# Kernel optimization log

Measured on AMD Instinct MI355X. Metric: run time of the kernel, lower is better.

Reference implementation:

```python
import jax, jax.numpy as jnp
import numpy as np

B, N_HIST, N_PRED = 32, 12, 12
N_NODE, INPUT_DIM, OUTPUT_DIM = 325, 2, 1
HIDDEN, N_RNN_LAYERS = 256, 2
EDGE_DIM, NODE_DIM, ORDER = 2, 64, 2
K = ORDER * EDGE_DIM + 1  # number of concat blocks per GraphConv


def setup_inputs() -> dict:
    key = jax.random.key(0)
    ks = iter(jax.random.split(key, 40))

    def rn(shape, s=0.05):
        return jax.random.normal(next(ks), shape, jnp.float32) * s

    L, H = N_RNN_LAYERS, HIDDEN
    d = {}
    d['inputs'] = jax.random.normal(next(ks), (B, N_HIST, N_NODE, INPUT_DIM), jnp.float32)
    d['vertexes'] = rn((N_NODE, NODE_DIM), 1.0)
    d['arcs_w0'] = rn((2 * NODE_DIM, 4 * NODE_DIM)); d['arcs_b0'] = jnp.zeros((4 * NODE_DIM,), jnp.float32)
    d['arcs_w1'] = rn((4 * NODE_DIM, 4 * NODE_DIM)); d['arcs_b1'] = jnp.zeros((4 * NODE_DIM,), jnp.float32)
    d['arcs_w2'] = rn((4 * NODE_DIM, EDGE_DIM)); d['arcs_b2'] = jnp.zeros((EDGE_DIM,), jnp.float32)
    d['enc_pre_w0'] = rn((K * INPUT_DIM, H)); d['enc_pre_b0'] = jnp.zeros((H,), jnp.float32)
    d['enc_pre_w1'] = rn((K * H, H)); d['enc_pre_b1'] = jnp.zeros((H,), jnp.float32)
    d['enc_wih'] = rn((L, 4 * H, H)); d['enc_whh'] = rn((L, 4 * H, H))
    d['enc_bih'] = jnp.zeros((L, 4 * H), jnp.float32); d['enc_bhh'] = jnp.zeros((L, 4 * H), jnp.float32)
    d['dec_pre_w0'] = rn((K * OUTPUT_DIM, H)); d['dec_pre_b0'] = jnp.zeros((H,), jnp.float32)
    d['dec_pre_w1'] = rn((K * H, H)); d['dec_pre_b1'] = jnp.zeros((H,), jnp.float32)
    d['dec_wih'] = rn((L, 4 * H, H)); d['dec_whh'] = rn((L, 4 * H, H))
    d['dec_bih'] = jnp.zeros((L, 4 * H), jnp.float32); d['dec_bhh'] = jnp.zeros((L, 4 * H), jnp.float32)
    d['dec_post_w0'] = rn((K * H, H)); d['dec_post_b0'] = jnp.zeros((H,), jnp.float32)
    d['dec_post_w1'] = rn((K * H, H)); d['dec_post_b1'] = jnp.zeros((H,), jnp.float32)
    d['proj_w'] = rn((H, OUTPUT_DIM)); d['proj_b'] = jnp.zeros((OUTPUT_DIM,), jnp.float32)
    return d


def _graph_conv(x, supports, w, b):
    out = [x]
    for e in range(supports.shape[0]):
        a = supports[e]
        x1 = x
        for _ in range(ORDER):
            x1 = jnp.einsum('...vc,vw->...wc', x1, a)
            out.append(x1)
    return jnp.concatenate(out, -1) @ w + b


def _stacked_gc(x, supports, layers):
    for w, b in layers:
        x = jax.nn.relu(_graph_conv(x, supports, w, b))
    return x


def _lstm_step(x, h, c, wih, whh, bih, bhh):
    # x: [BN, H]; h, c: [L, BN, H]; torch gate order i, f, g, o
    new_h, new_c = [], []
    for l in range(N_RNN_LAYERS):
        gates = x @ wih[l].T + bih[l] + h[l] @ whh[l].T + bhh[l]
        i, f, g, o = jnp.split(gates, 4, axis=-1)
        cn = jax.nn.sigmoid(f) * c[l] + jax.nn.sigmoid(i) * jnp.tanh(g)
        hn = jax.nn.sigmoid(o) * jnp.tanh(cn)
        new_h.append(hn); new_c.append(cn)
        x = hn
    return x, jnp.stack(new_h), jnp.stack(new_c)


def _adaptive_supports(vertexes, arcs_w0, arcs_b0, arcs_w1, arcs_b1, arcs_w2, arcs_b2):
    n = vertexes.shape[0]
    src = jnp.broadcast_to(vertexes[None, :, :], (n, n, NODE_DIM))
    dst = jnp.broadcast_to(vertexes[:, None, :], (n, n, NODE_DIM))
    h = jnp.concatenate([src, dst], -1)
    h = jax.nn.leaky_relu(h @ arcs_w0 + arcs_b0)
    h = jax.nn.leaky_relu(h @ arcs_w1 + arcs_b1)
    adj = jnp.transpose(h @ arcs_w2 + arcs_b2, (2, 0, 1))  # [E, N, N]
    adj = jax.nn.relu(adj)
    adj = adj / jnp.maximum(jnp.sum(jnp.abs(adj), axis=2, keepdims=True), 1e-12)
    # FAITHFUL to source: adj is computed but the function returns identity.expand(adj.shape)
    return jnp.broadcast_to(jnp.eye(n, dtype=jnp.float32)[None], adj.shape)


def _forward(inputs, vertexes, arcs_w0, arcs_b0, arcs_w1, arcs_b1, arcs_w2, arcs_b2,
             enc_pre_w0, enc_pre_b0, enc_pre_w1, enc_pre_b1,
             enc_wih, enc_whh, enc_bih, enc_bhh,
             dec_pre_w0, dec_pre_b0, dec_pre_w1, dec_pre_b1,
             dec_wih, dec_whh, dec_bih, dec_bhh,
             dec_post_w0, dec_post_b0, dec_post_w1, dec_post_b1,
             proj_w, proj_b):
    b, t, n, _ = inputs.shape
    H, L = HIDDEN, N_RNN_LAYERS
    supports = _adaptive_supports(vertexes, arcs_w0, arcs_b0, arcs_w1, arcs_b1, arcs_w2, arcs_b2)

    # ---- encoding ----
    x = _stacked_gc(inputs, supports, [(enc_pre_w0, enc_pre_b0), (enc_pre_w1, enc_pre_b1)])  # [B,T,N,H]
    seq = jnp.transpose(x, (1, 0, 2, 3)).reshape(t, b * n, H)
    h0 = jnp.zeros((L, b * n, H), inputs.dtype)
    c0 = jnp.zeros((L, b * n, H), inputs.dtype)

    def enc_step(carry, xt):
        hh, cc = carry
        _, hh, cc = _lstm_step(xt, hh, cc, enc_wih, enc_whh, enc_bih, enc_bhh)
        return (hh, cc), None

    (h, c), _ = jax.lax.scan(enc_step, (h0, c0), seq)
    # NOTE: source calls torch.dropout but discards the result -> no-op; reproduced by omission.

    dec_in0 = jnp.zeros((b, n, OUTPUT_DIM), inputs.dtype)
    dec_pre = [(dec_pre_w0, dec_pre_b0), (dec_pre_w1, dec_pre_b1)]
    dec_post = [(dec_post_w0, dec_post_b0), (dec_post_w1, dec_post_b1)]

    def dec_step(carry, _):
        x, hh, cc = carry
        x = _stacked_gc(x, supports, dec_pre)                      # [B,N,H]
        xf, hh, cc = _lstm_step(x.reshape(b * n, H), hh, cc, dec_wih, dec_whh, dec_bih, dec_bhh)
        x = _stacked_gc(xf.reshape(b, n, H), supports, dec_post)   # [B,N,H]
        out = x @ proj_w + proj_b                                  # [B,N,out_dim]
        return (out, hh, cc), out

    _, outs = jax.lax.scan(dec_step, (dec_in0, h, c), None, length=N_PRED)
    return jnp.transpose(outs, (1, 0, 2, 3))  # [B, n_pred, N, output_dim]


def reference(inputs, vertexes, arcs_w0, arcs_b0, arcs_w1, arcs_b1, arcs_w2, arcs_b2,
              enc_pre_w0, enc_pre_b0, enc_pre_w1, enc_pre_b1,
              enc_wih, enc_whh, enc_bih, enc_bhh,
              dec_pre_w0, dec_pre_b0, dec_pre_w1, dec_pre_b1,
              dec_wih, dec_whh, dec_bih, dec_bhh,
              dec_post_w0, dec_post_b0, dec_post_w1, dec_post_b1,
              proj_w, proj_b):
    return _forward(inputs, vertexes, arcs_w0, arcs_b0, arcs_w1, arcs_b1, arcs_w2, arcs_b2,
                    enc_pre_w0, enc_pre_b0, enc_pre_w1, enc_pre_b1,
                    enc_wih, enc_whh, enc_bih, enc_bhh,
                    dec_pre_w0, dec_pre_b0, dec_pre_w1, dec_pre_b1,
                    dec_wih, dec_whh, dec_bih, dec_bhh,
                    dec_post_w0, dec_post_b0, dec_post_w1, dec_post_b1,
                    proj_w, proj_b)
```

## Files before the change

kernel.cpp:

```cpp
#include <hip/hip_runtime.h>
#include <math.h>

#define BATCH 32
#define NNODE 325
#define T_HIST 12
#define T_PRED 12
#define H 256
#define G4 1024
#define ROWS (BATCH*NNODE)
#define MPAD 10496

typedef __attribute__((ext_vector_type(8))) short bf16x8;
typedef __attribute__((ext_vector_type(4))) float f32x4;
typedef unsigned short ushort_t;
typedef unsigned int uint_t;

#define GLL16(gp, sp) __builtin_amdgcn_global_load_lds( \
    (const __attribute__((address_space(1))) void*)(gp), \
    (__attribute__((address_space(3))) void*)(sp), 16, 0, 0)

__device__ inline float bf2f(ushort_t u) { return __uint_as_float(((uint_t)u) << 16); }

__device__ inline void split2(float v, ushort_t& h, ushort_t& l) {
    uint_t b = __float_as_uint(v);
    uint_t hb = (b + 0x7fffu + ((b >> 16) & 1u)) & 0xffff0000u;
    h = (ushort_t)(hb >> 16);
    float r = v - __uint_as_float(hb);
    uint_t rb = __float_as_uint(r);
    l = (ushort_t)((rb + 0x7fffu + ((rb >> 16) & 1u)) >> 16);
}

__device__ inline float sigm(float x) {
    x = fminf(fmaxf(x, -30.f), 30.f);
    return 1.f / (1.f + __expf(-x));
}
__device__ inline float tanh_f(float x) {
    x = fminf(fmaxf(x, -15.f), 15.f);
    float e = __expf(2.f * x);
    return (e - 1.f) / (e + 1.f);
}

__global__ void collapse_kernel(const float* __restrict__ w, float* __restrict__ out,
                                int cin, int nblk) {
    int idx = blockIdx.x * blockDim.x + threadIdx.x;
    if (idx >= cin * H) return;
    int c = idx / H, h = idx % H;
    float s = 0.f;
    for (int k = 0; k < nblk; ++k) s += w[(size_t)(k * cin + c) * H + h];
    out[idx] = s;
}

__global__ void pack_big_kernel(const float* __restrict__ wih, const float* __restrict__ whh,
                                const float* __restrict__ bih, const float* __restrict__ bhh,
                                ushort_t* __restrict__ Bxh, ushort_t* __restrict__ Bxl,
                                ushort_t* __restrict__ Bhh, ushort_t* __restrict__ Bhl,
                                float* __restrict__ biasI) {
    int idx = blockIdx.x * blockDim.x + threadIdx.x;
    if (idx >= 32 * G4) return;
    int kg = idx >> 10, col = idx & 1023;
    int j = col >> 2, g = col & 3;
    int gcol = g * 256 + j;
    if (kg == 0) biasI[col] = bih[gcol] + bhh[gcol];
#pragma unroll
    for (int jj = 0; jj < 8; ++jj) {
        int k = kg * 8 + jj;
        ushort_t hh, ll;
        split2(wih[(size_t)gcol * H + k], hh, ll);
        Bxh[(size_t)idx * 8 + jj] = hh; Bxl[(size_t)idx * 8 + jj] = ll;
        split2(whh[(size_t)gcol * H + k], hh, ll);
        Bhh[(size_t)idx * 8 + jj] = hh; Bhl[(size_t)idx * 8 + jj] = ll;
    }
}

__global__ void pack_small_kernel(const float* __restrict__ w,
                                  ushort_t* __restrict__ Bh, ushort_t* __restrict__ Bl) {
    int idx = blockIdx.x * blockDim.x + threadIdx.x;
    if (idx >= 32 * H) return;
    int kg = idx >> 8, n = idx & 255;
#pragma unroll
    for (int jj = 0; jj < 8; ++jj) {
        int k = kg * 8 + jj;
        float s = 0.f;
        for (int blk = 0; blk < 5; ++blk) s += w[(size_t)(blk * H + k) * H + n];
        ushort_t hh, ll; split2(s, hh, ll);
        Bh[(size_t)idx * 8 + jj] = hh; Bl[(size_t)idx * 8 + jj] = ll;
    }
}

__global__ void enc_pre0_pk(const float* __restrict__ inp, const float* __restrict__ w,
                            const float* __restrict__ b, ushort_t* __restrict__ oh,
                            ushort_t* __restrict__ ol, int t) {
    int m = blockIdx.x * 256 + threadIdx.x;
    int kg = blockIdx.y;
    float ip0 = 0.f, ip1 = 0.f;
    if (m < ROWS) {
        int bb = m / NNODE, nn = m % NNODE;
        const float* ip = inp + (((size_t)bb * T_HIST + t) * NNODE + nn) * 2;
        ip0 = ip[0]; ip1 = ip[1];
    }
    union { ushort_t u[8]; bf16x8 v; } hc, lc;
#pragma unroll
    for (int jj = 0; jj < 8; ++jj) {
        int j = kg * 8 + jj;
        float v = (m < ROWS) ? fmaxf(ip0 * w[j] + ip1 * w[H + j] + b[j], 0.f) : 0.f;
        split2(v, hc.u[jj], lc.u[jj]);
    }
    size_t base = ((size_t)kg * MPAD + m) * 8;
    *(bf16x8*)&oh[base] = hc.v;
    *(bf16x8*)&ol[base] = lc.v;
}

__global__ void dec_pre0_pk(const float* __restrict__ y, const float* __restrict__ w,
                            const float* __restrict__ b, ushort_t* __restrict__ oh,
                            ushort_t* __restrict__ ol) {
    int m = blockIdx.x * 256 + threadIdx.x;
    int kg = blockIdx.y;
    float yv = y[m];
    union { ushort_t u[8]; bf16x8 v; } hc, lc;
#pragma unroll
    for (int jj = 0; jj < 8; ++jj) {
        int j = kg * 8 + jj;
        float v = fmaxf(yv * w[j] + b[j], 0.f);
        split2(v, hc.u[jj], lc.u[jj]);
    }
    size_t base = ((size_t)kg * MPAD + m) * 8;
    *(bf16x8*)&oh[base] = hc.v;
    *(bf16x8*)&ol[base] = lc.v;
}

template<bool GATES, int NSC, int HSC, int NB>
__global__ __launch_bounds__(256, 2) void gemm_k(
    const ushort_t* __restrict__ AxH, const ushort_t* __restrict__ AxL,
    const ushort_t* __restrict__ AhH, const ushort_t* __restrict__ AhL,
    int astrideX, int arowX, int astrideH,
    const ushort_t* __restrict__ BxH, const ushort_t* __restrict__ BxL,
    const ushort_t* __restrict__ BhH, const ushort_t* __restrict__ BhL,
    const float* __restrict__ bias, float* __restrict__ cst,
    ushort_t* __restrict__ OH, ushort_t* __restrict__ OL,
    int ostride, int nbx, int doSwz)
{
    __shared__ __align__(16) ushort_t As[2][2][4096];
    __shared__ __align__(16) ushort_t Bs[2][2][4096];

    int bid = blockIdx.x;
    if (doSwz) { int cpx = gridDim.x >> 3; bid = (bid & 7) * cpx + (bid >> 3); }
    const int bm = (bid / nbx) * 128, bn = (bid % nbx) * 128;
    const int tid = threadIdx.x, lane = tid & 63, wid = tid >> 6;
    const int wm = wid >> 1, wn = wid & 1;
    const int l15 = lane & 15, lk = lane >> 4;

    auto stageSC = [&](int s, int slot) {
        const ushort_t *Ah, *Al, *Bh, *Bl; int ck, astr, abase;
        if (s < HSC) { Ah = AxH; Al = AxL; Bh = BxH; Bl = BxL; ck = s; astr = astrideX; abase = arowX; }
        else         { Ah = AhH; Al = AhL; Bh = BhH; Bl = BhL; ck = s - HSC; astr = astrideH; abase = 0; }
#pragma unroll
        for (int q = 0; q < 2; ++q) {
            int ubase = (tid & 192) + q * 256;
            int u = ubase + lane;
            int kgl = u >> 7, rc = u & 127;
            size_t ga = ((size_t)(ck * 4 + kgl) * astr + abase + bm + rc) * 8;
            size_t gb = ((size_t)(ck * 4 + kgl) * NB + bn + rc) * 8;
            GLL16(Ah + ga, &As[slot][0][ubase * 8]);
            GLL16(Al + ga, &As[slot][1][ubase * 8]);
            GLL16(Bh + gb, &Bs[slot][0][ubase * 8]);
            GLL16(Bl + gb, &Bs[slot][1][ubase * 8]);
        }
    };

    f32x4 acc[4][4] = {};

    stageSC(0, 0);

#pragma unroll
    for (int s = 0; s < NSC; ++s) {
        __builtin_amdgcn_s_barrier();
        if (s + 1 < NSC) {
            stageSC(s + 1, (s + 1) & 1);
            asm volatile("s_waitcnt vmcnt(8)" ::: "memory");
        } else {
            asm volatile("s_waitcnt vmcnt(0)" ::: "memory");
        }
        __builtin_amdgcn_s_barrier();
        __builtin_amdgcn_sched_barrier(0);

        const int slot = s & 1;
        bf16x8 ah[4], al[4], bh[4], bl[4];
#pragma unroll
        for (int i = 0; i < 4; ++i) {
            int ea = (lk * 128 + wm * 64 + i * 16 + l15) * 8;
            ah[i] = *(const bf16x8*)&As[slot][0][ea];
            al[i] = *(const bf16x8*)&As[slot][1][ea];
            int eb = (lk * 128 + wn * 64 + i * 16 + l15) * 8;
            bh[i] = *(const bf16x8*)&Bs[slot][0][eb];
            bl[i] = *(const bf16x8*)&Bs[slot][1][eb];
        }
#pragma unroll
        for (int i = 0; i < 4; ++i)
#pragma unroll
            for (int j = 0; j < 4; ++j)
                acc[i][j] = __builtin_amdgcn_mfma_f32_16x16x32_bf16(bh[j], ah[i], acc[i][j], 0, 0, 0);
#pragma unroll
        for (int i = 0; i < 4; ++i)
#pragma unroll
            for (int j = 0; j < 4; ++j)
                acc[i][j] = __builtin_amdgcn_mfma_f32_16x16x32_bf16(bl[j], ah[i], acc[i][j], 0, 0, 0);
#pragma unroll
        for (int i = 0; i < 4; ++i)
#pragma unroll
            for (int j = 0; j < 4; ++j)
                acc[i][j] = __builtin_amdgcn_mfma_f32_16x16x32_bf16(bh[j], al[i], acc[i][j], 0, 0, 0);
    }

    if constexpr (GATES) {
        uint_t* Hs = (uint_t*)(&As[0][0][0]);
        const int jbase = (bn >> 2) + wn * 16;
#pragma unroll
        for (int jj = 0; jj < 4; ++jj) {
            float4 b4 = *(const float4*)&bias[bn + wn * 64 + jj * 16 + lk * 4];
            int j = jbase + jj * 4 + lk;
#pragma unroll
            for (int i = 0; i < 4; ++i) {
                int m = bm + wm * 64 + i * 16 + l15;
                float vi = acc[i][jj][0] + b4.x;
                float vf = acc[i][jj][1] + b4.y;
                float vg = acc[i][jj][2] + b4.z;
                float vo = acc[i][jj][3] + b4.w;
                float cold = cst[(size_t)j * MPAD + m];
                float cn = sigm(vf) * cold + sigm(vi) * tanh_f(vg);
                float hn = sigm(vo) * tanh_f(cn);
                cst[(size_t)j * MPAD + m] = cn;
                ushort_t hh, hl; split2(hn, hh, hl);
                Hs[(wm * 64 + i * 16 + l15) * 36 + wn * 16 + jj * 4 + lk] = ((uint_t)hh << 16) | hl;
            }
        }
        __syncthreads();
#pragma unroll
        for (int it = 0; it < 2; ++it) {
            int u = tid + it * 256;
            int mloc = u & 127, kgl = u >> 7;
            uint4 w0 = *(const uint4*)&Hs[mloc * 36 + kgl * 8];
            uint4 w1 = *(const uint4*)&Hs[mloc * 36 + kgl * 8 + 4];
            union { uint_t u2[4]; bf16x8 v; } hi, lo;
            hi.u2[0] = (w0.x >> 16) | (w0.y & 0xffff0000u);
            hi.u2[1] = (w0.z >> 16) | (w0.w & 0xffff0000u);
            hi.u2[2] = (w1.x >> 16) | (w1.y & 0xffff0000u);
            hi.u2[3] = (w1.z >> 16) | (w1.w & 0xffff0000u);
            lo.u2[0] = (w0.x & 0xffffu) | (w0.y << 16);
            lo.u2[1] = (w0.z & 0xffffu) | (w0.w << 16);
            lo.u2[2] = (w1.x & 0xffffu) | (w1.y << 16);
            lo.u2[3] = (w1.z & 0xffffu) | (w1.w << 16);
            size_t base = ((size_t)((bn >> 5) + kgl) * ostride + bm + mloc) * 8;
            *(bf16x8*)&OH[base] = hi.v;
            *(bf16x8*)&OL[base] = lo.v;
        }
    } else {
#pragma unroll
        for (int jj = 0; jj < 4; ++jj) {
            float4 b4 = *(const float4*)&bias[bn + wn * 64 + jj * 16 + lk * 4];
#pragma unroll
            for (int i = 0; i < 4; ++i) {
                float v0 = fmaxf(acc[i][jj][0] + b4.x, 0.f);
                float v1 = fmaxf(acc[i][jj][1] + b4.y, 0.f);
                float v2 = fmaxf(acc[i][jj][2] + b4.z, 0.f);
                float v3 = fmaxf(acc[i][jj][3] + b4.w, 0.f);
                ushort_t h0, h1, h2, h3, l0, l1, l2, l3;
                split2(v0, h0, l0); split2(v1, h1, l1);
                split2(v2, h2, l2); split2(v3, h3, l3);
                uint_t hu0 = (uint_t)h0 | ((uint_t)h1 << 16), hu1 = (uint_t)h2 | ((uint_t)h3 << 16);
                uint_t lu0 = (uint_t)l0 | ((uint_t)l1 << 16), lu1 = (uint_t)l2 | ((uint_t)l3 << 16);
                uint_t ph0 = (uint_t)__shfl_xor((int)hu0, 16, 64);
                uint_t ph1 = (uint_t)__shfl_xor((int)hu1, 16, 64);
                uint_t pl0 = (uint_t)__shfl_xor((int)lu0, 16, 64);
                uint_t pl1 = (uint_t)__shfl_xor((int)lu1, 16, 64);
                int kgg = ((bn + wn * 64 + jj * 16) >> 3) + (lk >> 1);
                size_t base = ((size_t)kgg * ostride + bm + wm * 64 + i * 16 + l15) * 8;
                union { uint_t u2[4]; bf16x8 v; } ch;
                if ((lk & 1) == 0) {
                    ch.u2[0] = hu0; ch.u2[1] = hu1; ch.u2[2] = ph0; ch.u2[3] = ph1;
                    *(bf16x8*)&OH[base] = ch.v;
                } else {
                    ch.u2[0] = pl0; ch.u2[1] = pl1; ch.u2[2] = lu0; ch.u2[3] = lu1;
                    *(bf16x8*)&OL[base] = ch.v;
                }
            }
        }
    }
}

__global__ void proj_kernel(const ushort_t* __restrict__ xh, const ushort_t* __restrict__ xl,
                            const float* __restrict__ pw, const float* __restrict__ pb,
                            float* __restrict__ y, float* __restrict__ out, int t) {
    int wid = threadIdx.x >> 6, lane = threadIdx.x & 63;
    int r = blockIdx.x * 4 + wid;
    if (r >= ROWS) return;
    const int kg = lane >> 1, sub = (lane & 1) * 4;
    size_t base = ((size_t)kg * MPAD + r) * 8 + sub;
    float s = 0.f;
#pragma unroll
    for (int q = 0; q < 4; ++q) {
        int k = kg * 8 + sub + q;
        s += (bf2f(xh[base + q]) + bf2f(xl[base + q])) * pw[k];
    }
#pragma unroll
    for (int off = 32; off > 0; off >>= 1) s += __shfl_down(s, off, 64);
    if (lane == 0) {
        float v = s + pb[0];
        y[r] = v;
        int bb = r / NNODE, n = r % NNODE;
        out[((size_t)bb * T_PRED + t) * NNODE + n] = v;
    }
}

static inline void gemm_big(const ushort_t* xH, const ushort_t* xL,
                            const ushort_t* hH, const ushort_t* hL,
                            ushort_t* const* B, const float* bias, float* c,
                            ushort_t* oH, ushort_t* oL, hipStream_t s) {
    gemm_k<true, 16, 8, 1024><<<656, 256, 0, s>>>(
        xH, xL, hH, hL, MPAD, 0, MPAD,
        B[0], B[1], B[2], B[3], bias, c, oH, oL, MPAD, 8, 1);
}
static inline void gemm_small(const ushort_t* aH, const ushort_t* aL,
                              const ushort_t* bH, const ushort_t* bL, const float* bias,
                              ushort_t* oH, ushort_t* oL, hipStream_t s) {
    gemm_k<false, 8, 8, 256><<<164, 256, 0, s>>>(
        aH, aL, nullptr, nullptr, MPAD, 0, MPAD,
        bH, bL, nullptr, nullptr, bias, nullptr, oH, oL, MPAD, 2, 0);
}

extern "C" void kernel_launch(void* const* d_in, const int* in_sizes, int n_in,
                              void* d_out, int out_size, void* d_ws, size_t ws_size,
                              hipStream_t stream) {
    (void)in_sizes; (void)n_in; (void)out_size; (void)ws_size;

    const float* inputs      = (const float*)d_in[0];
    const float* enc_pre_w0  = (const float*)d_in[8];
    const float* enc_pre_b0  = (const float*)d_in[9];
    const float* enc_pre_w1  = (const float*)d_in[10];
    const float* enc_pre_b1  = (const float*)d_in[11];
    const float* enc_wih     = (const float*)d_in[12];
    const float* enc_whh     = (const float*)d_in[13];
    const float* enc_bih     = (const float*)d_in[14];
    const float* enc_bhh     = (const float*)d_in[15];
    const float* dec_pre_w0  = (const float*)d_in[16];
    const float* dec_pre_b0  = (const float*)d_in[17];
    const float* dec_pre_w1  = (const float*)d_in[18];
    const float* dec_pre_b1  = (const float*)d_in[19];
    const float* dec_wih     = (const float*)d_in[20];
    const float* dec_whh     = (const float*)d_in[21];
    const float* dec_bih     = (const float*)d_in[22];
    const float* dec_bhh     = (const float*)d_in[23];
    const float* dec_post_w0 = (const float*)d_in[24];
    const float* dec_post_b0 = (const float*)d_in[25];
    const float* dec_post_w1 = (const float*)d_in[26];
    const float* dec_post_b1 = (const float*)d_in[27];
    const float* proj_w      = (const float*)d_in[28];
    const float* proj_b      = (const float*)d_in[29];
    float* out = (float*)d_out;

    char* wsb = (char*)d_ws;
    size_t off = 0;
    auto allocF = [&](size_t n) { float* p = (float*)(wsb + off); off += ((n * 4 + 15) & ~(size_t)15); return p; };
    auto allocU = [&](size_t n) { ushort_t* p = (ushort_t*)(wsb + off); off += ((n * 2 + 15) & ~(size_t)15); return p; };

    const size_t BIGW = (size_t)32 * G4 * 8;
    const size_t SMLW = (size_t)32 * H * 8;
    const size_t ACT  = (size_t)32 * MPAD * 8;

    ushort_t* eB0[4]; ushort_t* eB1[4]; ushort_t* dB0[4]; ushort_t* dB1[4];
    for (int q = 0; q < 4; ++q) eB0[q] = allocU(BIGW);
    for (int q = 0; q < 4; ++q) eB1[q] = allocU(BIGW);
    for (int q = 0; q < 4; ++q) dB0[q] = allocU(BIGW);
    for (int q = 0; q < 4; ++q) dB1[q] = allocU(BIGW);
    float* eBI0 = allocF(G4); float* eBI1 = allocF(G4);
    float* dBI0 = allocF(G4); float* dBI1 = allocF(G4);
    ushort_t* eP1h = allocU(SMLW); ushort_t* eP1l = allocU(SMLW);
    ushort_t* dP1h = allocU(SMLW); ushort_t* dP1l = allocU(SMLW);
    ushort_t* po0h = allocU(SMLW); ushort_t* po0l = allocU(SMLW);
    ushort_t* po1h = allocU(SMLW); ushort_t* po1l = allocU(SMLW);
    float* encW0eff = allocF(2 * H);
    float* decPre0eff = allocF(H);
    ushort_t* h0H[2]; ushort_t* h0L[2]; ushort_t* h1H[2]; ushort_t* h1L[2];
    for (int q = 0; q < 2; ++q) { h0H[q] = allocU(ACT); h0L[q] = allocU(ACT); }
    for (int q = 0; q < 2; ++q) { h1H[q] = allocU(ACT); h1L[q] = allocU(ACT); }
    float* c0 = allocF((size_t)H * MPAD);
    float* c1 = allocF((size_t)H * MPAD);
    ushort_t* xaH = allocU(ACT); ushort_t* xaL = allocU(ACT);
    ushort_t* xbH = allocU(ACT); ushort_t* xbL = allocU(ACT);
    float* y = allocF(MPAD);

    const size_t LOFF = (size_t)G4 * H;
    const int EW = 256;

    pack_big_kernel<<<128, EW, 0, stream>>>(enc_wih, enc_whh, enc_bih, enc_bhh,
                                            eB0[0], eB0[1], eB0[2], eB0[3], eBI0);
    pack_big_kernel<<<128, EW, 0, stream>>>(enc_wih + LOFF, enc_whh + LOFF, enc_bih + G4, enc_bhh + G4,
                                            eB1[0], eB1[1], eB1[2], eB1[3], eBI1);
    pack_big_kernel<<<128, EW, 0, stream>>>(dec_wih, dec_whh, dec_bih, dec_bhh,
                                            dB0[0], dB0[1], dB0[2], dB0[3], dBI0);
    pack_big_kernel<<<128, EW, 0, stream>>>(dec_wih + LOFF, dec_whh + LOFF, dec_bih + G4, dec_bhh + G4,
                                            dB1[0], dB1[1], dB1[2], dB1[3], dBI1);
    pack_small_kernel<<<32, EW, 0, stream>>>(enc_pre_w1, eP1h, eP1l);
    pack_small_kernel<<<32, EW, 0, stream>>>(dec_pre_w1, dP1h, dP1l);
    pack_small_kernel<<<32, EW, 0, stream>>>(dec_post_w0, po0h, po0l);
    pack_small_kernel<<<32, EW, 0, stream>>>(dec_post_w1, po1h, po1l);
    collapse_kernel<<<2, EW, 0, stream>>>(enc_pre_w0, encW0eff, 2, 5);
    collapse_kernel<<<1, EW, 0, stream>>>(dec_pre_w0, decPre0eff, 1, 5);

    for (int q = 0; q < 2; ++q) {
        hipMemsetAsync(h0H[q], 0, ACT * 2, stream); hipMemsetAsync(h0L[q], 0, ACT * 2, stream);
        hipMemsetAsync(h1H[q], 0, ACT * 2, stream); hipMemsetAsync(h1L[q], 0, ACT * 2, stream);
    }
    hipMemsetAsync(c0, 0, (size_t)H * MPAD * 4, stream);
    hipMemsetAsync(c1, 0, (size_t)H * MPAD * 4, stream);
    hipMemsetAsync(y, 0, (size_t)MPAD * 4, stream);

    const dim3 PG(MPAD / 256, 32);

    for (int t = 0; t < T_HIST; ++t) {
        int pr = t & 1;
        enc_pre0_pk<<<PG, EW, 0, stream>>>(inputs, encW0eff, enc_pre_b0, xaH, xaL, t);
        gemm_small(xaH, xaL, eP1h, eP1l, enc_pre_b1, xbH, xbL, stream);
        gemm_big(xbH, xbL, h0H[pr], h0L[pr], eB0, eBI0, c0, h0H[pr ^ 1], h0L[pr ^ 1], stream);
        gemm_big(h0H[pr ^ 1], h0L[pr ^ 1], h1H[pr], h1L[pr], eB1, eBI1, c1, h1H[pr ^ 1], h1L[pr ^ 1], stream);
    }

    for (int d = 0; d < T_PRED; ++d) {
        int pr = d & 1;
        dec_pre0_pk<<<PG, EW, 0, stream>>>(y, decPre0eff, dec_pre_b0, xaH, xaL);
        gemm_small(xaH, xaL, dP1h, dP1l, dec_pre_b1, xbH, xbL, stream);
        gemm_big(xbH, xbL, h0H[pr], h0L[pr], dB0, dBI0, c0, h0H[pr ^ 1], h0L[pr ^ 1], stream);
        gemm_big(h0H[pr ^ 1], h0L[pr ^ 1], h1H[pr], h1L[pr], dB1, dBI1, c1, h1H[pr ^ 1], h1L[pr ^ 1], stream);
        gemm_small(h1H[pr ^ 1], h1L[pr ^ 1], po0h, po0l, dec_post_b0, xaH, xaL, stream);
        gemm_small(xaH, xaL, po1h, po1l, dec_post_b1, xbH, xbL, stream);
        proj_kernel<<<(ROWS + 3) / 4, EW, 0, stream>>>(xbH, xbL, proj_w, proj_b, y, out, d);
    }
}
```

Baseline: 2.601 ms.

## Switch GEMM to 32x32x16 MFMA, narrow small-GEMM N tile, direct gate epilogue

The split-bf16 GEMM now uses 32x32x16 MFMA tiles in place of 16x16x32, which changes fragment loads and accumulator layout. The LSTM gate epilogue now writes h directly through lane shuffles and no longer goes through an LDS transpose with __syncthreads. The small GEMM uses a 64-wide N tile with double the blocks, swizzle enabled and min 3 waves per EU, to raise occupancy. The main cost targeted is MFMA issue overhead and the epilogue sync; s_setprio is added around the MFMA blocks. The risks are higher register pressure from 16-wide accumulators and partial (8-byte) stores in the non-gate epilogue.

New measurement: 2.777 ms. +6.8%, slower.

```diff
diff --git a/kernel.cpp b/kernel.cpp
--- a/kernel.cpp
+++ b/kernel.cpp
@@ -11,7 +11,7 @@
 #define MPAD 10496
 
 typedef __attribute__((ext_vector_type(8))) short bf16x8;
-typedef __attribute__((ext_vector_type(4))) float f32x4;
+typedef __attribute__((ext_vector_type(16))) float f32x16;
 typedef unsigned short ushort_t;
 typedef unsigned int uint_t;
 
@@ -128,46 +128,55 @@
     *(bf16x8*)&ol[base] = lc.v;
 }
 
-template<bool GATES, int NSC, int HSC, int NB>
-__global__ __launch_bounds__(256, 2) void gemm_k(
+template<bool GATES, int NSC, int HSC, int BNT, int NBG, int MINW>
+__global__ __launch_bounds__(256, MINW) void gemm_k(
     const ushort_t* __restrict__ AxH, const ushort_t* __restrict__ AxL,
     const ushort_t* __restrict__ AhH, const ushort_t* __restrict__ AhL,
-    int astrideX, int arowX, int astrideH,
     const ushort_t* __restrict__ BxH, const ushort_t* __restrict__ BxL,
     const ushort_t* __restrict__ BhH, const ushort_t* __restrict__ BhL,
     const float* __restrict__ bias, float* __restrict__ cst,
     ushort_t* __restrict__ OH, ushort_t* __restrict__ OL,
-    int ostride, int nbx, int doSwz)
+    int nbx, int doSwz)
 {
-    __shared__ __align__(16) ushort_t As[2][2][4096];
-    __shared__ __align__(16) ushort_t Bs[2][2][4096];
+    constexpr int ACH = 512;
+    constexpr int BCH = BNT * 4;
+    constexpr int BU = BCH / 256;
+    constexpr int JB = BNT / 64;
+    __shared__ __align__(16) ushort_t As[2][2][ACH * 8];
+    __shared__ __align__(16) ushort_t Bs[2][2][BCH * 8];
 
     int bid = blockIdx.x;
     if (doSwz) { int cpx = gridDim.x >> 3; bid = (bid & 7) * cpx + (bid >> 3); }
-    const int bm = (bid / nbx) * 128, bn = (bid % nbx) * 128;
+    const int bm = (bid / nbx) * 128, bn = (bid % nbx) * BNT;
     const int tid = threadIdx.x, lane = tid & 63, wid = tid >> 6;
     const int wm = wid >> 1, wn = wid & 1;
-    const int l15 = lane & 15, lk = lane >> 4;
+    const int l31 = lane & 31, hi = lane >> 5;
 
     auto stageSC = [&](int s, int slot) {
-        const ushort_t *Ah, *Al, *Bh, *Bl; int ck, astr, abase;
-        if (s < HSC) { Ah = AxH; Al = AxL; Bh = BxH; Bl = BxL; ck = s; astr = astrideX; abase = arowX; }
-        else         { Ah = AhH; Al = AhL; Bh = BhH; Bl = BhL; ck = s - HSC; astr = astrideH; abase = 0; }
+        const ushort_t *Ah, *Al, *Bh, *Bl; int ck;
+        if (s < HSC) { Ah = AxH; Al = AxL; Bh = BxH; Bl = BxL; ck = s; }
+        else         { Ah = AhH; Al = AhL; Bh = BhH; Bl = BhL; ck = s - HSC; }
 #pragma unroll
         for (int q = 0; q < 2; ++q) {
             int ubase = (tid & 192) + q * 256;
             int u = ubase + lane;
             int kgl = u >> 7, rc = u & 127;
-            size_t ga = ((size_t)(ck * 4 + kgl) * astr + abase + bm + rc) * 8;
-            size_t gb = ((size_t)(ck * 4 + kgl) * NB + bn + rc) * 8;
+            size_t ga = ((size_t)(ck * 4 + kgl) * MPAD + bm + rc) * 8;
             GLL16(Ah + ga, &As[slot][0][ubase * 8]);
             GLL16(Al + ga, &As[slot][1][ubase * 8]);
+        }
+#pragma unroll
+        for (int q = 0; q < BU; ++q) {
+            int ubase = (tid & 192) + q * 256;
+            int u = ubase + lane;
+            int kgl = u / BNT, nc = u % BNT;
+            size_t gb = ((size_t)(ck * 4 + kgl) * NBG + bn + nc) * 8;
             GLL16(Bh + gb, &Bs[slot][0][ubase * 8]);
             GLL16(Bl + gb, &Bs[slot][1][ubase * 8]);
         }
     };
 
-    f32x4 acc[4][4] = {};
+    f32x16 acc[2][JB] = {};
 
     stageSC(0, 0);
 
@@ -176,7 +185,8 @@
         __builtin_amdgcn_s_barrier();
         if (s + 1 < NSC) {
             stageSC(s + 1, (s + 1) & 1);
-            asm volatile("s_waitcnt vmcnt(8)" ::: "memory");
+            if constexpr (BU == 2) asm volatile("s_waitcnt vmcnt(8)" ::: "memory");
+            else                   asm volatile("s_waitcnt vmcnt(6)" ::: "memory");
         } else {
             asm volatile("s_waitcnt vmcnt(0)" ::: "memory");
         }
@@ -184,104 +194,120 @@
         __builtin_amdgcn_sched_barrier(0);
 
         const int slot = s & 1;
-        bf16x8 ah[4], al[4], bh[4], bl[4];
-#pragma unroll
-        for (int i = 0; i < 4; ++i) {
-            int ea = (lk * 128 + wm * 64 + i * 16 + l15) * 8;
-            ah[i] = *(const bf16x8*)&As[slot][0][ea];
-            al[i] = *(const bf16x8*)&As[slot][1][ea];
-            int eb = (lk * 128 + wn * 64 + i * 16 + l15) * 8;
-            bh[i] = *(const bf16x8*)&Bs[slot][0][eb];
-            bl[i] = *(const bf16x8*)&Bs[slot][1][eb];
-        }
-#pragma unroll
-        for (int i = 0; i < 4; ++i)
-#pragma unroll
-            for (int j = 0; j < 4; ++j)
-                acc[i][j] = __builtin_amdgcn_mfma_f32_16x16x32_bf16(bh[j], ah[i], acc[i][j], 0, 0, 0);
-#pragma unroll
-        for (int i = 0; i < 4; ++i)
-#pragma unroll
-            for (int j = 0; j < 4; ++j)
-                acc[i][j] = __builtin_amdgcn_mfma_f32_16x16x32_bf16(bl[j], ah[i], acc[i][j], 0, 0, 0);
-#pragma unroll
-        for (int i = 0; i < 4; ++i)
-#pragma unroll
-            for (int j = 0; j < 4; ++j)
-                acc[i][j] = __builtin_amdgcn_mfma_f32_16x16x32_bf16(bh[j], al[i], acc[i][j], 0, 0, 0);
+        bf16x8 afh[2][2], afl[2][2], bfh[2][JB], bfl[2][JB];
+#pragma unroll
+        for (int kh = 0; kh < 2; ++kh) {
+#pragma unroll
+            for (int i = 0; i < 2; ++i) {
+                int ca = ((2 * kh + hi) * 128 + wm * 64 + i * 32 + l31) * 8;
+                afh[kh][i] = *(const bf16x8*)&As[slot][0][ca];
+                afl[kh][i] = *(const bf16x8*)&As[slot][1][ca];
+            }
+#pragma unroll
+            for (int j = 0; j < JB; ++j) {
+                int cb = ((2 * kh + hi) * BNT + wn * (BNT / 2) + j * 32 + l31) * 8;
+                bfh[kh][j] = *(const bf16x8*)&Bs[slot][0][cb];
+                bfl[kh][j] = *(const bf16x8*)&Bs[slot][1][cb];
+            }
+        }
+        __builtin_amdgcn_s_setprio(1);
+#pragma unroll
+        for (int kh = 0; kh < 2; ++kh) {
+#pragma unroll
+            for (int i = 0; i < 2; ++i)
+#pragma unroll
+                for (int j = 0; j < JB; ++j)
+                    acc[i][j] = __builtin_amdgcn_mfma_f32_32x32x16_bf16(bfh[kh][j], afh[kh][i], acc[i][j], 0, 0, 0);
+#pragma unroll
+            for (int i = 0; i < 2; ++i)
+#pragma unroll
+                for (int j = 0; j < JB; ++j)
+                    acc[i][j] = __builtin_amdgcn_mfma_f32_32x32x16_bf16(bfl[kh][j], afh[kh][i], acc[i][j], 0, 0, 0);
+#pragma unroll
+            for (int i = 0; i < 2; ++i)
+#pragma unroll
+                for (int j = 0; j < JB; ++j)
+                    acc[i][j] = __builtin_amdgcn_mfma_f32_32x32x16_bf16(bfh[kh][j], afl[kh][i], acc[i][j], 0, 0, 0);
+        }
+        __builtin_amdgcn_s_setprio(0);
     }
 
     if constexpr (GATES) {
-        uint_t* Hs = (uint_t*)(&As[0][0][0]);
+        float4 b4[2][4];
+#pragma unroll
+        for (int jj = 0; jj < 2; ++jj)
+#pragma unroll
+            for (int q = 0; q < 4; ++q)
+                b4[jj][q] = *(const float4*)&bias[bn + wn * 64 + jj * 32 + 8 * q + 4 * hi];
         const int jbase = (bn >> 2) + wn * 16;
 #pragma unroll
-        for (int jj = 0; jj < 4; ++jj) {
-            float4 b4 = *(const float4*)&bias[bn + wn * 64 + jj * 16 + lk * 4];
-            int j = jbase + jj * 4 + lk;
-#pragma unroll
-            for (int i = 0; i < 4; ++i) {
-                int m = bm + wm * 64 + i * 16 + l15;
-                float vi = acc[i][jj][0] + b4.x;
-                float vf = acc[i][jj][1] + b4.y;
-                float vg = acc[i][jj][2] + b4.z;
-                float vo = acc[i][jj][3] + b4.w;
-                float cold = cst[(size_t)j * MPAD + m];
-                float cn = sigm(vf) * cold + sigm(vi) * tanh_f(vg);
-                float hn = sigm(vo) * tanh_f(cn);
-                cst[(size_t)j * MPAD + m] = cn;
-                ushort_t hh, hl; split2(hn, hh, hl);
-                Hs[(wm * 64 + i * 16 + l15) * 36 + wn * 16 + jj * 4 + lk] = ((uint_t)hh << 16) | hl;
+        for (int i = 0; i < 2; ++i) {
+            int m = bm + wm * 64 + i * 32 + l31;
+#pragma unroll
+            for (int jj = 0; jj < 2; ++jj) {
+                ushort_t hhq[4], hlq[4];
+#pragma unroll
+                for (int q = 0; q < 4; ++q) {
+                    float vi = acc[i][jj][4 * q + 0] + b4[jj][q].x;
+                    float vf = acc[i][jj][4 * q + 1] + b4[jj][q].y;
+                    float vg = acc[i][jj][4 * q + 2] + b4[jj][q].z;
+                    float vo = acc[i][jj][4 * q + 3] + b4[jj][q].w;
+                    int j = jbase + jj * 8 + 2 * q + hi;
+                    size_t ci = (size_t)j * MPAD + m;
+                    float cold = cst[ci];
+                    float cn = sigm(vf) * cold + sigm(vi) * tanh_f(vg);
+                    float hn = sigm(vo) * tanh_f(cn);
+                    cst[ci] = cn;
+                    split2(hn, hhq[q], hlq[q]);
+                }
+                uint_t mh0 = (uint_t)hhq[0] | ((uint_t)hhq[1] << 16);
+                uint_t mh1 = (uint_t)hhq[2] | ((uint_t)hhq[3] << 16);
+                uint_t ml0 = (uint_t)hlq[0] | ((uint_t)hlq[1] << 16);
+                uint_t ml1 = (uint_t)hlq[2] | ((uint_t)hlq[3] << 16);
+                uint_t ph0 = (uint_t)__shfl_xor((int)mh0, 32, 64);
+                uint_t ph1 = (uint_t)__shfl_xor((int)mh1, 32, 64);
+                uint_t pl0 = (uint_t)__shfl_xor((int)ml0, 32, 64);
+                uint_t pl1 = (uint_t)__shfl_xor((int)ml1, 32, 64);
+                int kg = (bn >> 5) + wn * 2 + jj;
+                size_t base = ((size_t)kg * MPAD + m) * 8;
+                if (hi == 0) {
+                    uint4 w;
+                    w.x = (mh0 & 0xffffu) | (ph0 << 16);
+                    w.y = (mh0 >> 16) | (ph0 & 0xffff0000u);
+                    w.z = (mh1 & 0xffffu) | (ph1 << 16);
+                    w.w = (mh1 >> 16) | (ph1 & 0xffff0000u);
+                    *(uint4*)&OH[base] = w;
+                } else {
+                    uint4 w;
+                    w.x = (pl0 & 0xffffu) | (ml0 << 16);
+                    w.y = (pl0 >> 16) | (ml0 & 0xffff0000u);
+                    w.z = (pl1 & 0xffffu) | (ml1 << 16);
+                    w.w = (pl1 >> 16) | (ml1 & 0xffff0000u);
+                    *(uint4*)&OL[base] = w;
+                }
             }
         }
-        __syncthreads();
-#pragma unroll
-        for (int it = 0; it < 2; ++it) {
-            int u = tid + it * 256;
-            int mloc = u & 127, kgl = u >> 7;
-            uint4 w0 = *(const uint4*)&Hs[mloc * 36 + kgl * 8];
-            uint4 w1 = *(const uint4*)&Hs[mloc * 36 + kgl * 8 + 4];
-            union { uint_t u2[4]; bf16x8 v; } hi, lo;
-            hi.u2[0] = (w0.x >> 16) | (w0.y & 0xffff0000u);
-            hi.u2[1] = (w0.z >> 16) | (w0.w & 0xffff0000u);
-            hi.u2[2] = (w1.x >> 16) | (w1.y & 0xffff0000u);
-            hi.u2[3] = (w1.z >> 16) | (w1.w & 0xffff0000u);
-            lo.u2[0] = (w0.x & 0xffffu) | (w0.y << 16);
-            lo.u2[1] = (w0.z & 0xffffu) | (w0.w << 16);
-            lo.u2[2] = (w1.x & 0xffffu) | (w1.y << 16);
-            lo.u2[3] = (w1.z & 0xffffu) | (w1.w << 16);
-            size_t base = ((size_t)((bn >> 5) + kgl) * ostride + bm + mloc) * 8;
-            *(bf16x8*)&OH[base] = hi.v;
-            *(bf16x8*)&OL[base] = lo.v;
-        }
     } else {
 #pragma unroll
-        for (int jj = 0; jj < 4; ++jj) {
-            float4 b4 = *(const float4*)&bias[bn + wn * 64 + jj * 16 + lk * 4];
-#pragma unroll
-            for (int i = 0; i < 4; ++i) {
-                float v0 = fmaxf(acc[i][jj][0] + b4.x, 0.f);
-                float v1 = fmaxf(acc[i][jj][1] + b4.y, 0.f);
-                float v2 = fmaxf(acc[i][jj][2] + b4.z, 0.f);
-                float v3 = fmaxf(acc[i][jj][3] + b4.w, 0.f);
+        for (int i = 0; i < 2; ++i) {
+            int m = bm + wm * 64 + i * 32 + l31;
+#pragma unroll
+            for (int q = 0; q < 4; ++q) {
+                float4 b4 = *(const float4*)&bias[bn + wn * (BNT / 2) + 8 * q + 4 * hi];
+                float v0 = fmaxf(acc[i][0][4 * q + 0] + b4.x, 0.f);
+                float v1 = fmaxf(acc[i][0][4 * q + 1] + b4.y, 0.f);
+                float v2 = fmaxf(acc[i][0][4 * q + 2] + b4.z, 0.f);
+                float v3 = fmaxf(acc[i][0][4 * q + 3] + b4.w, 0.f);
                 ushort_t h0, h1, h2, h3, l0, l1, l2, l3;
                 split2(v0, h0, l0); split2(v1, h1, l1);
                 split2(v2, h2, l2); split2(v3, h3, l3);
-                uint_t hu0 = (uint_t)h0 | ((uint_t)h1 << 16), hu1 = (uint_t)h2 | ((uint_t)h3 << 16);
-                uint_t lu0 = (uint_t)l0 | ((uint_t)l1 << 16), lu1 = (uint_t)l2 | ((uint_t)l3 << 16);
-                uint_t ph0 = (uint_t)__shfl_xor((int)hu0, 16, 64);
-                uint_t ph1 = (uint_t)__shfl_xor((int)hu1, 16, 64);
-                uint_t pl0 = (uint_t)__shfl_xor((int)lu0, 16, 64);
-                uint_t pl1 = (uint_t)__shfl_xor((int)lu1, 16, 64);
-                int kgg = ((bn + wn * 64 + jj * 16) >> 3) + (lk >> 1);
-                size_t base = ((size_t)kgg * ostride + bm + wm * 64 + i * 16 + l15) * 8;
-                union { uint_t u2[4]; bf16x8 v; } ch;
-                if ((lk & 1) == 0) {
-                    ch.u2[0] = hu0; ch.u2[1] = hu1; ch.u2[2] = ph0; ch.u2[3] = ph1;
-                    *(bf16x8*)&OH[base] = ch.v;
-                } else {
-                    ch.u2[0] = pl0; ch.u2[1] = pl1; ch.u2[2] = lu0; ch.u2[3] = lu1;
-                    *(bf16x8*)&OL[base] = ch.v;
-                }
+                int kg = (bn >> 3) + wn * (BNT / 16) + q;
+                size_t base = ((size_t)kg * MPAD + m) * 8 + 4 * hi;
+                uint2 wh, wl;
+                wh.x = (uint_t)h0 | ((uint_t)h1 << 16); wh.y = (uint_t)h2 | ((uint_t)h3 << 16);
+                wl.x = (uint_t)l0 | ((uint_t)l1 << 16); wl.y = (uint_t)l2 | ((uint_t)l3 << 16);
+                *(uint2*)&OH[base] = wh;
+                *(uint2*)&OL[base] = wl;
             }
         }
     }
@@ -315,16 +341,14 @@
                             const ushort_t* hH, const ushort_t* hL,
                             ushort_t* const* B, const float* bias, float* c,
                             ushort_t* oH, ushort_t* oL, hipStream_t s) {
-    gemm_k<true, 16, 8, 1024><<<656, 256, 0, s>>>(
-        xH, xL, hH, hL, MPAD, 0, MPAD,
-        B[0], B[1], B[2], B[3], bias, c, oH, oL, MPAD, 8, 1);
+    gemm_k<true, 16, 8, 128, 1024, 2><<<656, 256, 0, s>>>(
+        xH, xL, hH, hL, B[0], B[1], B[2], B[3], bias, c, oH, oL, 8, 1);
 }
 static inline void gemm_small(const ushort_t* aH, const ushort_t* aL,
                               const ushort_t* bH, const ushort_t* bL, const float* bias,
                               ushort_t* oH, ushort_t* oL, hipStream_t s) {
-    gemm_k<false, 8, 8, 256><<<164, 256, 0, s>>>(
-        aH, aL, nullptr, nullptr, MPAD, 0, MPAD,
-        bH, bL, nullptr, nullptr, bias, nullptr, oH, oL, MPAD, 2, 0);
+    gemm_k<false, 8, 8, 64, 256, 3><<<328, 256, 0, s>>>(
+        aH, aL, aH, aL, bH, bL, bH, bL, bias, nullptr, oH, oL, 4, 1);
 }
 
 extern "C" void kernel_launch(void* const* d_in, const int* in_sizes, int n_in,
```

## Narrow GEMM N-tile to 64 for more blocks and higher occupancy

Applied to the files above, without the earlier changes.

The templated GEMM now uses a 128x64 block tile instead of 128x128. Each wave holds half as many accumulators, the B staging buffer shrinks, and launch bounds allow 3 blocks per CU. Both the gate GEMM and the small GEMM are launched with many more blocks (1312 and 328) so the CUs are better filled. The gate epilogue is rewritten around a narrower padded LDS transpose, and the small GEMM now enables block swizzling. In exchange, each block reuses its A tile across fewer output columns, so A is loaded from global memory twice as often.

Result: faster. 2.447 ms (-5.9%).

```diff
diff --git a/kernel.cpp b/kernel.cpp
--- a/kernel.cpp
+++ b/kernel.cpp
@@ -128,46 +128,52 @@
     *(bf16x8*)&ol[base] = lc.v;
 }
 
-template<bool GATES, int NSC, int HSC, int NB>
-__global__ __launch_bounds__(256, 2) void gemm_k(
+template<bool GATES, int NSC, int HSC, int BNT, int NBG, int MINW>
+__global__ __launch_bounds__(256, MINW) void gemm_k(
     const ushort_t* __restrict__ AxH, const ushort_t* __restrict__ AxL,
     const ushort_t* __restrict__ AhH, const ushort_t* __restrict__ AhL,
-    int astrideX, int arowX, int astrideH,
     const ushort_t* __restrict__ BxH, const ushort_t* __restrict__ BxL,
     const ushort_t* __restrict__ BhH, const ushort_t* __restrict__ BhL,
     const float* __restrict__ bias, float* __restrict__ cst,
     ushort_t* __restrict__ OH, ushort_t* __restrict__ OL,
-    int ostride, int nbx, int doSwz)
+    int nbx, int doSwz)
 {
+    constexpr int BCH = BNT * 4;
+    constexpr int JB  = BNT / 32;
     __shared__ __align__(16) ushort_t As[2][2][4096];
-    __shared__ __align__(16) ushort_t Bs[2][2][4096];
+    __shared__ __align__(16) ushort_t Bs[2][2][BCH * 8];
 
     int bid = blockIdx.x;
     if (doSwz) { int cpx = gridDim.x >> 3; bid = (bid & 7) * cpx + (bid >> 3); }
-    const int bm = (bid / nbx) * 128, bn = (bid % nbx) * 128;
-    const int tid = threadIdx.x, lane = tid & 63, wid = tid >> 6;
-    const int wm = wid >> 1, wn = wid & 1;
+    const int bm = (bid / nbx) * 128, bn = (bid % nbx) * BNT;
+    const int tid = threadIdx.x, lane = tid & 63;
+    const int wm = (tid >> 7) & 1, wn = (tid >> 6) & 1;
     const int l15 = lane & 15, lk = lane >> 4;
 
     auto stageSC = [&](int s, int slot) {
-        const ushort_t *Ah, *Al, *Bh, *Bl; int ck, astr, abase;
-        if (s < HSC) { Ah = AxH; Al = AxL; Bh = BxH; Bl = BxL; ck = s; astr = astrideX; abase = arowX; }
-        else         { Ah = AhH; Al = AhL; Bh = BhH; Bl = BhL; ck = s - HSC; astr = astrideH; abase = 0; }
+        const ushort_t *Ah, *Al, *Bh, *Bl; int ck;
+        if (s < HSC) { Ah = AxH; Al = AxL; Bh = BxH; Bl = BxL; ck = s; }
+        else         { Ah = AhH; Al = AhL; Bh = BhH; Bl = BhL; ck = s - HSC; }
 #pragma unroll
         for (int q = 0; q < 2; ++q) {
             int ubase = (tid & 192) + q * 256;
             int u = ubase + lane;
             int kgl = u >> 7, rc = u & 127;
-            size_t ga = ((size_t)(ck * 4 + kgl) * astr + abase + bm + rc) * 8;
-            size_t gb = ((size_t)(ck * 4 + kgl) * NB + bn + rc) * 8;
+            size_t ga = ((size_t)(ck * 4 + kgl) * MPAD + bm + rc) * 8;
             GLL16(Ah + ga, &As[slot][0][ubase * 8]);
             GLL16(Al + ga, &As[slot][1][ubase * 8]);
+        }
+        {
+            int ubase = tid & 192;
+            int u = tid;
+            int kgl = u >> 6, nc = u & 63;
+            size_t gb = ((size_t)(ck * 4 + kgl) * NBG + bn + nc) * 8;
             GLL16(Bh + gb, &Bs[slot][0][ubase * 8]);
             GLL16(Bl + gb, &Bs[slot][1][ubase * 8]);
         }
     };
 
-    f32x4 acc[4][4] = {};
+    f32x4 acc[4][JB] = {};
 
     stageSC(0, 0);
 
@@ -176,7 +182,7 @@
         __builtin_amdgcn_s_barrier();
         if (s + 1 < NSC) {
             stageSC(s + 1, (s + 1) & 1);
-            asm volatile("s_waitcnt vmcnt(8)" ::: "memory");
+            asm volatile("s_waitcnt vmcnt(6)" ::: "memory");
         } else {
             asm volatile("s_waitcnt vmcnt(0)" ::: "memory");
         }
@@ -184,85 +190,83 @@
         __builtin_amdgcn_sched_barrier(0);
 
         const int slot = s & 1;
-        bf16x8 ah[4], al[4], bh[4], bl[4];
+        bf16x8 ah[4], al[4], bh[JB], bl[JB];
 #pragma unroll
         for (int i = 0; i < 4; ++i) {
             int ea = (lk * 128 + wm * 64 + i * 16 + l15) * 8;
             ah[i] = *(const bf16x8*)&As[slot][0][ea];
             al[i] = *(const bf16x8*)&As[slot][1][ea];
-            int eb = (lk * 128 + wn * 64 + i * 16 + l15) * 8;
-            bh[i] = *(const bf16x8*)&Bs[slot][0][eb];
-            bl[i] = *(const bf16x8*)&Bs[slot][1][eb];
+        }
+#pragma unroll
+        for (int j = 0; j < JB; ++j) {
+            int eb = (lk * BNT + wn * (BNT / 2) + j * 16 + l15) * 8;
+            bh[j] = *(const bf16x8*)&Bs[slot][0][eb];
+            bl[j] = *(const bf16x8*)&Bs[slot][1][eb];
         }
 #pragma unroll
         for (int i = 0; i < 4; ++i)
 #pragma unroll
-            for (int j = 0; j < 4; ++j)
+            for (int j = 0; j < JB; ++j)
                 acc[i][j] = __builtin_amdgcn_mfma_f32_16x16x32_bf16(bh[j], ah[i], acc[i][j], 0, 0, 0);
 #pragma unroll
         for (int i = 0; i < 4; ++i)
 #pragma unroll
-            for (int j = 0; j < 4; ++j)
+            for (int j = 0; j < JB; ++j)
                 acc[i][j] = __builtin_amdgcn_mfma_f32_16x16x32_bf16(bl[j], ah[i], acc[i][j], 0, 0, 0);
 #pragma unroll
         for (int i = 0; i < 4; ++i)
 #pragma unroll
-            for (int j = 0; j < 4; ++j)
+            for (int j = 0; j < JB; ++j)
                 acc[i][j] = __builtin_amdgcn_mfma_f32_16x16x32_bf16(bh[j], al[i], acc[i][j], 0, 0, 0);
     }
 
     if constexpr (GATES) {
-        uint_t* Hs = (uint_t*)(&As[0][0][0]);
-        const int jbase = (bn >> 2) + wn * 16;
-#pragma unroll
-        for (int jj = 0; jj < 4; ++jj) {
-            float4 b4 = *(const float4*)&bias[bn + wn * 64 + jj * 16 + lk * 4];
-            int j = jbase + jj * 4 + lk;
+        uint_t* Hs = (uint_t*)&As[0][0][0];
+        const int jb0 = (bn >> 2) + wn * 8;
+#pragma unroll
+        for (int j = 0; j < JB; ++j) {
+            float4 b4 = *(const float4*)&bias[bn + wn * 32 + j * 16 + lk * 4];
+            int cell = jb0 + j * 4 + lk;
 #pragma unroll
             for (int i = 0; i < 4; ++i) {
                 int m = bm + wm * 64 + i * 16 + l15;
-                float vi = acc[i][jj][0] + b4.x;
-                float vf = acc[i][jj][1] + b4.y;
-                float vg = acc[i][jj][2] + b4.z;
-                float vo = acc[i][jj][3] + b4.w;
-                float cold = cst[(size_t)j * MPAD + m];
+                float vi = acc[i][j][0] + b4.x;
+                float vf = acc[i][j][1] + b4.y;
+                float vg = acc[i][j][2] + b4.z;
+                float vo = acc[i][j][3] + b4.w;
+                size_t ci = (size_t)cell * MPAD + m;
+                float cold = cst[ci];
                 float cn = sigm(vf) * cold + sigm(vi) * tanh_f(vg);
                 float hn = sigm(vo) * tanh_f(cn);
-                cst[(size_t)j * MPAD + m] = cn;
+                cst[ci] = cn;
                 ushort_t hh, hl; split2(hn, hh, hl);
-                Hs[(wm * 64 + i * 16 + l15) * 36 + wn * 16 + jj * 4 + lk] = ((uint_t)hh << 16) | hl;
+                Hs[(wm * 64 + i * 16 + l15) * 17 + wn * 8 + j * 4 + lk] = ((uint_t)hh << 16) | hl;
             }
         }
         __syncthreads();
-#pragma unroll
-        for (int it = 0; it < 2; ++it) {
-            int u = tid + it * 256;
-            int mloc = u & 127, kgl = u >> 7;
-            uint4 w0 = *(const uint4*)&Hs[mloc * 36 + kgl * 8];
-            uint4 w1 = *(const uint4*)&Hs[mloc * 36 + kgl * 8 + 4];
-            union { uint_t u2[4]; bf16x8 v; } hi, lo;
-            hi.u2[0] = (w0.x >> 16) | (w0.y & 0xffff0000u);
-            hi.u2[1] = (w0.z >> 16) | (w0.w & 0xffff0000u);
-            hi.u2[2] = (w1.x >> 16) | (w1.y & 0xffff0000u);
-            hi.u2[3] = (w1.z >> 16) | (w1.w & 0xffff0000u);
-            lo.u2[0] = (w0.x & 0xffffu) | (w0.y << 16);
-            lo.u2[1] = (w0.z & 0xffffu) | (w0.w << 16);
-            lo.u2[2] = (w1.x & 0xffffu) | (w1.y << 16);
-            lo.u2[3] = (w1.z & 0xffffu) | (w1.w << 16);
-            size_t base = ((size_t)((bn >> 5) + kgl) * ostride + bm + mloc) * 8;
+        {
+            int mloc = tid & 127, kgl = tid >> 7;
+            union { ushort_t u[8]; bf16x8 v; } hi, lo;
+#pragma unroll
+            for (int jj = 0; jj < 8; ++jj) {
+                uint_t wv = Hs[mloc * 17 + kgl * 8 + jj];
+                hi.u[jj] = (ushort_t)(wv >> 16);
+                lo.u[jj] = (ushort_t)(wv & 0xffffu);
+            }
+            size_t base = ((size_t)((bn >> 5) + kgl) * MPAD + bm + mloc) * 8;
             *(bf16x8*)&OH[base] = hi.v;
             *(bf16x8*)&OL[base] = lo.v;
         }
     } else {
 #pragma unroll
-        for (int jj = 0; jj < 4; ++jj) {
-            float4 b4 = *(const float4*)&bias[bn + wn * 64 + jj * 16 + lk * 4];
+        for (int j = 0; j < JB; ++j) {
+            float4 b4 = *(const float4*)&bias[bn + wn * (BNT / 2) + j * 16 + lk * 4];
 #pragma unroll
             for (int i = 0; i < 4; ++i) {
-                float v0 = fmaxf(acc[i][jj][0] + b4.x, 0.f);
-                float v1 = fmaxf(acc[i][jj][1] + b4.y, 0.f);
-                float v2 = fmaxf(acc[i][jj][2] + b4.z, 0.f);
-                float v3 = fmaxf(acc[i][jj][3] + b4.w, 0.f);
+                float v0 = fmaxf(acc[i][j][0] + b4.x, 0.f);
+                float v1 = fmaxf(acc[i][j][1] + b4.y, 0.f);
+                float v2 = fmaxf(acc[i][j][2] + b4.z, 0.f);
+                float v3 = fmaxf(acc[i][j][3] + b4.w, 0.f);
                 ushort_t h0, h1, h2, h3, l0, l1, l2, l3;
                 split2(v0, h0, l0); split2(v1, h1, l1);
                 split2(v2, h2, l2); split2(v3, h3, l3);
@@ -272,8 +276,8 @@
                 uint_t ph1 = (uint_t)__shfl_xor((int)hu1, 16, 64);
                 uint_t pl0 = (uint_t)__shfl_xor((int)lu0, 16, 64);
                 uint_t pl1 = (uint_t)__shfl_xor((int)lu1, 16, 64);
-                int kgg = ((bn + wn * 64 + jj * 16) >> 3) + (lk >> 1);
-                size_t base = ((size_t)kgg * ostride + bm + wm * 64 + i * 16 + l15) * 8;
+                int kgg = ((bn + wn * (BNT / 2) + j * 16) >> 3) + (lk >> 1);
+                size_t base = ((size_t)kgg * MPAD + bm + wm * 64 + i * 16 + l15) * 8;
                 union { uint_t u2[4]; bf16x8 v; } ch;
                 if ((lk & 1) == 0) {
                     ch.u2[0] = hu0; ch.u2[1] = hu1; ch.u2[2] = ph0; ch.u2[3] = ph1;
@@ -315,16 +319,14 @@
                             const ushort_t* hH, const ushort_t* hL,
                             ushort_t* const* B, const float* bias, float* c,
                             ushort_t* oH, ushort_t* oL, hipStream_t s) {
-    gemm_k<true, 16, 8, 1024><<<656, 256, 0, s>>>(
-        xH, xL, hH, hL, MPAD, 0, MPAD,
-        B[0], B[1], B[2], B[3], bias, c, oH, oL, MPAD, 8, 1);
+    gemm_k<true, 16, 8, 64, 1024, 3><<<82 * 16, 256, 0, s>>>(
+        xH, xL, hH, hL, B[0], B[1], B[2], B[3], bias, c, oH, oL, 16, 1);
 }
 static inline void gemm_small(const ushort_t* aH, const ushort_t* aL,
                               const ushort_t* bH, const ushort_t* bL, const float* bias,
                               ushort_t* oH, ushort_t* oL, hipStream_t s) {
-    gemm_k<false, 8, 8, 256><<<164, 256, 0, s>>>(
-        aH, aL, nullptr, nullptr, MPAD, 0, MPAD,
-        bH, bL, nullptr, nullptr, bias, nullptr, oH, oL, MPAD, 2, 0);
+    gemm_k<false, 8, 8, 64, 256, 3><<<82 * 4, 256, 0, s>>>(
+        aH, aL, aH, aL, bH, bL, bH, bL, bias, nullptr, oH, oL, 4, 1);
 }
 
 extern "C" void kernel_launch(void* const* d_in, const int* in_sizes, int n_in,
```
